# Performance work log

Hardware: AMD Instinct MI355X
Metric: run time of the kernel (lower is better)

The kernel has to match this reference:

```python
import jax, jax.numpy as jnp
import numpy as np

N_NODES = 50000
N_EDGES = 800000
IN_DIM = 256
HID = 32
HEADS = 8
OUT_DIM = 16
NEG_SLOPE = 0.2


def setup_inputs() -> dict:
    key = jax.random.key(0)
    ks = jax.random.split(key, 12)
    s = 0.05
    return {
        "emb": jax.random.normal(ks[0], (N_NODES, IN_DIM), jnp.float32),
        "src": jax.random.randint(ks[1], (N_EDGES,), 0, N_NODES),
        "dst": jax.random.randint(ks[2], (N_EDGES,), 0, N_NODES),
        "W1": jax.random.normal(ks[3], (IN_DIM, HEADS * HID), jnp.float32) * s,
        "attn_l1": jax.random.normal(ks[4], (HEADS, HID), jnp.float32) * s,
        "attn_r1": jax.random.normal(ks[5], (HEADS, HID), jnp.float32) * s,
        "bias1": jax.random.normal(ks[6], (HEADS * HID,), jnp.float32) * s,
        "W2": jax.random.normal(ks[7], (HEADS * HID, OUT_DIM), jnp.float32) * s,
        "attn_l2": jax.random.normal(ks[8], (1, OUT_DIM), jnp.float32) * s,
        "attn_r2": jax.random.normal(ks[9], (1, OUT_DIM), jnp.float32) * s,
        "bias2": jax.random.normal(ks[10], (OUT_DIM,), jnp.float32) * s,
    }


def gat_conv(x, src, dst, W, attn_l, attn_r, bias, n_heads, d_out):
    # x: [N, F_in] -> per-head projection h: [N, H, D]
    n = x.shape[0]
    h = (x @ W).reshape(n, n_heads, d_out)
    el = jnp.sum(h * attn_l, axis=-1)  # [N, H]
    er = jnp.sum(h * attn_r, axis=-1)  # [N, H]
    # edge scores with LeakyReLU (DGL negative_slope=0.2)
    e = jax.nn.leaky_relu(el[src] + er[dst], NEG_SLOPE)  # [E, H]
    # edge softmax over incoming edges of each destination node
    m = jax.ops.segment_max(e, dst, num_segments=n)  # [N, H]
    ee = jnp.exp(e - m[dst])
    denom = jax.ops.segment_sum(ee, dst, num_segments=n)  # [N, H]
    alpha = ee / denom[dst]  # [E, H]
    # weighted scatter-sum aggregation
    out = jax.ops.segment_sum(h[src] * alpha[:, :, None], dst, num_segments=n)  # [N, H, D]
    return out + bias.reshape(1, n_heads, d_out)


def reference(emb, src, dst, W1, attn_l1, attn_r1, bias1, W2, attn_l2, attn_r2, bias2):
    h = gat_conv(emb, src, dst, W1, attn_l1, attn_r1, bias1, HEADS, HID)  # [N, 8, 32]
    h = jax.nn.elu(h.reshape(N_NODES, HEADS * HID))  # [N, 256]
    out = gat_conv(h, src, dst, W2, attn_l2, attn_r2, bias2, 1, OUT_DIM)  # [N, 1, 16]
    return jnp.squeeze(out, axis=1)  # [N, 16]
```

## Files before the change

kernel.cpp:

```cpp
#include <hip/hip_runtime.h>
#include <math.h>

#define N_NODES 50000
#define N_EDGES 800000
#define NEG_SLOPE 0.2f

typedef __attribute__((ext_vector_type(8))) short bf16x8;
typedef __attribute__((ext_vector_type(4))) float f32x4;
typedef __attribute__((ext_vector_type(4))) _Float16 half4;

__device__ inline unsigned short f32_to_bf16_rn(float x) {
    unsigned u = __builtin_bit_cast(unsigned, x);
    unsigned r = u + 0x7fffu + ((u >> 16) & 1u);
    return (unsigned short)(r >> 16);
}
__device__ inline float bf16_bits_to_f32(unsigned short h) {
    unsigned u = ((unsigned)h) << 16;
    return __builtin_bit_cast(float, u);
}
__device__ inline void load_lds16(const void* g, void* l) {
    __builtin_amdgcn_global_load_lds(
        (const __attribute__((address_space(1))) void*)g,
        (__attribute__((address_space(3))) void*)l, 16, 0, 0);
}


__device__ __forceinline__ void count_body(int bb, const int* __restrict__ dst,
                                           int* __restrict__ deg) {
    int i = bb * 256 + threadIdx.x;
    if (i < N_EDGES) atomicAdd(&deg[dst[i]], 1);
}

__device__ __forceinline__ void convert_body(int n, const float* __restrict__ W,
                                             unsigned short* __restrict__ Th,
                                             unsigned short* __restrict__ Tl) {
    int k = threadIdx.x;
    float x = W[k * 256 + n];
    unsigned short h = f32_to_bf16_rn(x);
    float lo = x - bf16_bits_to_f32(h);
    size_t idx = ((size_t)(k >> 3) * 256 + n) * 8 + (k & 7);
    Th[idx] = h;
    Tl[idx] = f32_to_bf16_rn(lo);
}

__device__ __forceinline__ void assign_body(int bb, const int* __restrict__ deg,
                                            int* __restrict__ offs,
                                            int* __restrict__ cursor,
                                            int* __restrict__ gcounter) {
    __shared__ int buf[256];
    __shared__ int base;
    int tid = threadIdx.x;
    int v = bb * 256 + tid;
    int d = (v < N_NODES) ? deg[v] : 0;
    buf[tid] = d;
    __syncthreads();
    for (int off = 1; off < 256; off <<= 1) {
        int x = (tid >= off) ? buf[tid - off] : 0;
        __syncthreads();
        buf[tid] += x;
        __syncthreads();
    }
    if (tid == 255) base = atomicAdd(gcounter, buf[255]);
    __syncthreads();
    if (v < N_NODES) {
        int start = base + buf[tid] - d;
        offs[v] = start;
        cursor[v] = start;
    }
}

__device__ __forceinline__ void scatter_body(int bb, const int* __restrict__ src,
                                             const int* __restrict__ dst,
                                             int* __restrict__ cursor,
                                             int* __restrict__ src_csr) {
    int i = bb * 256 + threadIdx.x;
    if (i < N_EDGES) {
        int p = atomicAdd(&cursor[dst[i]], 1);
        src_csr[p] = src[i];
    }
}


__device__ __forceinline__ void gemm1_body(int bb, const float* __restrict__ A,
                                           const unsigned short* __restrict__ BTh,
                                           const unsigned short* __restrict__ BTl,
                                           const float* __restrict__ al,
                                           const float* __restrict__ ar,
                                           _Float16* __restrict__ C,
                                           float* __restrict__ el,
                                           float* __restrict__ er, int M) {
    __shared__ unsigned short Ah[4][64][8], Al[4][64][8];
    __shared__ unsigned short Bh[4][256][8], Bl[4][256][8];
    int tid = threadIdx.x;
    int lane = tid & 63, wave = tid >> 6;
    int kgl = lane >> 4, rl = lane & 15;
    int row0 = bb * 64;

    f32x4 acc[4][4];
#pragma unroll
    for (int i = 0; i < 4; i++)
#pragma unroll
        for (int j = 0; j < 4; j++) acc[i][j] = (f32x4){0.f, 0.f, 0.f, 0.f};

    int rowA = tid >> 2, kgA = tid & 3;
    int grA = row0 + rowA;
    const float* pA = &A[(size_t)grA * 256 + kgA * 8];
    float4 x0 = make_float4(0.f, 0.f, 0.f, 0.f);
    float4 x1 = make_float4(0.f, 0.f, 0.f, 0.f);
    if (grA < M) {
        x0 = *reinterpret_cast<const float4*>(pA);
        x1 = *reinterpret_cast<const float4*>(pA + 4);
    }

    for (int step = 0; step < 8; step++) {
        int k0 = step * 32;
        {
            float xs[8] = {x0.x, x0.y, x0.z, x0.w, x1.x, x1.y, x1.z, x1.w};
            unsigned short hs[8], ls[8];
#pragma unroll
            for (int j = 0; j < 8; j++) {
                hs[j] = f32_to_bf16_rn(xs[j]);
                ls[j] = f32_to_bf16_rn(xs[j] - bf16_bits_to_f32(hs[j]));
            }
            *reinterpret_cast<bf16x8*>(&Ah[kgA][rowA][0]) = *reinterpret_cast<bf16x8*>(hs);
            *reinterpret_cast<bf16x8*>(&Al[kgA][rowA][0]) = *reinterpret_cast<bf16x8*>(ls);
        }
        int s0 = k0 >> 3;
#pragma unroll
        for (int i = 0; i < 4; i++) {
            load_lds16(&BTh[((size_t)(s0 + i) * 256 + tid) * 8], &Bh[i][wave << 6][0]);
            load_lds16(&BTl[((size_t)(s0 + i) * 256 + tid) * 8], &Bl[i][wave << 6][0]);
        }
        __syncthreads();
        if (step < 7 && grA < M) {
            x0 = *reinterpret_cast<const float4*>(pA + (step + 1) * 32);
            x1 = *reinterpret_cast<const float4*>(pA + (step + 1) * 32 + 4);
        }
        bf16x8 a_h[4], a_l[4];
#pragma unroll
        for (int mf = 0; mf < 4; mf++) {
            int row = mf * 16 + rl;
            a_h[mf] = *reinterpret_cast<bf16x8*>(&Ah[kgl][row][0]);
            a_l[mf] = *reinterpret_cast<bf16x8*>(&Al[kgl][row][0]);
        }
#pragma unroll
        for (int nf = 0; nf < 4; nf++) {
            int col = wave * 64 + nf * 16 + rl;
            bf16x8 bh = *reinterpret_cast<bf16x8*>(&Bh[kgl][col][0]);
            bf16x8 bl = *reinterpret_cast<bf16x8*>(&Bl[kgl][col][0]);
#pragma unroll
            for (int mf = 0; mf < 4; mf++) {
                acc[mf][nf] = __builtin_amdgcn_mfma_f32_16x16x32_bf16(a_h[mf], bh, acc[mf][nf], 0, 0, 0);
                acc[mf][nf] = __builtin_amdgcn_mfma_f32_16x16x32_bf16(a_h[mf], bl, acc[mf][nf], 0, 0, 0);
                acc[mf][nf] = __builtin_amdgcn_mfma_f32_16x16x32_bf16(a_l[mf], bh, acc[mf][nf], 0, 0, 0);
            }
        }
        __syncthreads();
    }
    float alv[4], arv[4];
#pragma unroll
    for (int nf = 0; nf < 4; nf++) {
        int c = wave * 64 + nf * 16 + rl;
        alv[nf] = al[c];
        arv[nf] = ar[c];
    }
#pragma unroll
    for (int mf = 0; mf < 4; mf++) {
#pragma unroll
        for (int rr = 0; rr < 4; rr++) {
            int grow = row0 + mf * 16 + (lane >> 4) * 4 + rr;
            bool ok = grow < M;
            if (ok) {
#pragma unroll
                for (int nf = 0; nf < 4; nf++) {
                    int gcol = wave * 64 + nf * 16 + rl;
                    C[(size_t)grow * 256 + gcol] = (_Float16)acc[mf][nf][rr];
                }
            }
            float e0 = acc[mf][0][rr] * alv[0] + acc[mf][1][rr] * alv[1];
            float e1 = acc[mf][2][rr] * alv[2] + acc[mf][3][rr] * alv[3];
            float f0 = acc[mf][0][rr] * arv[0] + acc[mf][1][rr] * arv[1];
            float f1 = acc[mf][2][rr] * arv[2] + acc[mf][3][rr] * arv[3];
#pragma unroll
            for (int off = 8; off >= 1; off >>= 1) {
                e0 += __shfl_down(e0, off, 16);
                e1 += __shfl_down(e1, off, 16);
                f0 += __shfl_down(f0, off, 16);
                f1 += __shfl_down(f1, off, 16);
            }
            if (rl == 0 && ok) {
                int h0 = wave * 2;
                el[grow * 8 + h0] = e0;
                el[grow * 8 + h0 + 1] = e1;
                er[grow * 8 + h0] = f0;
                er[grow * 8 + h0 + 1] = f1;
            }
        }
    }
}


__global__ __launch_bounds__(256) void k_count_convert(const int* __restrict__ dst,
                                                       int* __restrict__ deg,
                                                       const float* __restrict__ W1,
                                                       unsigned short* __restrict__ Th,
                                                       unsigned short* __restrict__ Tl) {
    int b = blockIdx.x;
    if (b < 3125) count_body(b, dst, deg);
    else convert_body(b - 3125, W1, Th, Tl);
}

__global__ __launch_bounds__(256) void k_gemmA_assign(const float* __restrict__ A,
                                                      const unsigned short* __restrict__ BTh,
                                                      const unsigned short* __restrict__ BTl,
                                                      const float* __restrict__ al,
                                                      const float* __restrict__ ar,
                                                      _Float16* __restrict__ C,
                                                      float* __restrict__ el,
                                                      float* __restrict__ er, int M,
                                                      const int* __restrict__ deg,
                                                      int* __restrict__ offs,
                                                      int* __restrict__ cursor,
                                                      int* __restrict__ gcounter) {
    int b = blockIdx.x;
    if (b < 391) gemm1_body(b, A, BTh, BTl, al, ar, C, el, er, M);
    else assign_body(b - 391, deg, offs, cursor, gcounter);
}

__global__ __launch_bounds__(256) void k_gemmB_scatter(const float* __restrict__ A,
                                                       const unsigned short* __restrict__ BTh,
                                                       const unsigned short* __restrict__ BTl,
                                                       const float* __restrict__ al,
                                                       const float* __restrict__ ar,
                                                       _Float16* __restrict__ C,
                                                       float* __restrict__ el,
                                                       float* __restrict__ er, int M,
                                                       const int* __restrict__ src,
                                                       const int* __restrict__ dst,
                                                       int* __restrict__ cursor,
                                                       int* __restrict__ src_csr) {
    int b = blockIdx.x;
    if (b < 391) gemm1_body(391 + b, A, BTh, BTl, al, ar, C, el, er, M);
    else scatter_body(b - 391, src, dst, cursor, src_csr);
}


__global__ __launch_bounds__(64) void agg1_fused(const int* __restrict__ offs,
                                                 const int* __restrict__ deg_arr,
                                                 const int* __restrict__ src_csr,
                                                 const float* __restrict__ el,
                                                 const float* __restrict__ er,
                                                 const _Float16* __restrict__ h1h,
                                                 const float* __restrict__ bias1,
                                                 _Float16* __restrict__ x2) {
    __shared__ float sc[64][8];
    int v = blockIdx.x;
    int t = threadIdx.x;
    int head = t >> 3, slot = t & 7;
    int start = offs[v];
    int deg = deg_arr[v];
    int end = start + deg;
    int ncache = (deg < 64) ? deg : 64;
    float erv = er[v * 8 + head];
    float s = 0.f;
    for (int base = 0; base < ncache; base += 8) {
        int e = base + slot;
        if (e < ncache) {
            int u = src_csr[start + e];
            float x = el[u * 8 + head] + erv;
            x = (x >= 0.f) ? x : NEG_SLOPE * x;
            float ex = expf(x);
            sc[e][head] = ex;
            s += ex;
        }
    }
    for (int base = 64; base < deg; base += 8) {
        int e = base + slot;
        if (e < deg) {
            int u = src_csr[start + e];
            float x = el[u * 8 + head] + erv;
            x = (x >= 0.f) ? x : NEG_SLOPE * x;
            s += expf(x);
        }
    }
    s += __shfl_xor(s, 1);
    s += __shfl_xor(s, 2);
    s += __shfl_xor(s, 4);
    float invs = (s > 0.f) ? 1.f / s : 0.f;
    __syncthreads();
    float4 acc = make_float4(0.f, 0.f, 0.f, 0.f);
    int i = start;
    for (; i + 3 < end && (i - start) + 3 < 64; i += 4) {
        int e = i - start;
        int u0 = src_csr[i];
        int u1 = src_csr[i + 1];
        int u2 = src_csr[i + 2];
        int u3 = src_csr[i + 3];
        float a0 = sc[e][head] * invs;
        float a1 = sc[e + 1][head] * invs;
        float a2 = sc[e + 2][head] * invs;
        float a3 = sc[e + 3][head] * invs;
        half4 p0 = *reinterpret_cast<const half4*>(&h1h[(size_t)u0 * 256 + 4 * t]);
        half4 p1 = *reinterpret_cast<const half4*>(&h1h[(size_t)u1 * 256 + 4 * t]);
        half4 p2 = *reinterpret_cast<const half4*>(&h1h[(size_t)u2 * 256 + 4 * t]);
        half4 p3 = *reinterpret_cast<const half4*>(&h1h[(size_t)u3 * 256 + 4 * t]);
        acc.x += a0 * (float)p0[0] + a1 * (float)p1[0] + a2 * (float)p2[0] + a3 * (float)p3[0];
        acc.y += a0 * (float)p0[1] + a1 * (float)p1[1] + a2 * (float)p2[1] + a3 * (float)p3[1];
        acc.z += a0 * (float)p0[2] + a1 * (float)p1[2] + a2 * (float)p2[2] + a3 * (float)p3[2];
        acc.w += a0 * (float)p0[3] + a1 * (float)p1[3] + a2 * (float)p2[3] + a3 * (float)p3[3];
    }
    for (; i < end; i++) {
        int e = i - start;
        int u0 = src_csr[i];
        float a0;
        if (e < 64) {
            a0 = sc[e][head] * invs;
        } else {
            float x = el[u0 * 8 + head] + erv;
            x = (x >= 0.f) ? x : NEG_SLOPE * x;
            a0 = expf(x) * invs;
        }
        half4 p0 = *reinterpret_cast<const half4*>(&h1h[(size_t)u0 * 256 + 4 * t]);
        acc.x += a0 * (float)p0[0];
        acc.y += a0 * (float)p0[1];
        acc.z += a0 * (float)p0[2];
        acc.w += a0 * (float)p0[3];
    }
    float4 b = *reinterpret_cast<const float4*>(&bias1[4 * t]);
    float ox = acc.x + b.x, oy = acc.y + b.y, oz = acc.z + b.z, ow = acc.w + b.w;
    ox = (ox > 0.f) ? ox : (expf(ox) - 1.f);
    oy = (oy > 0.f) ? oy : (expf(oy) - 1.f);
    oz = (oz > 0.f) ? oz : (expf(oz) - 1.f);
    ow = (ow > 0.f) ? ow : (expf(ow) - 1.f);
    half4 o = {(_Float16)ox, (_Float16)oy, (_Float16)oz, (_Float16)ow};
    *reinterpret_cast<half4*>(&x2[(size_t)v * 256 + 4 * t]) = o;
}


__global__ __launch_bounds__(256) void gemm2_mfma(const _Float16* __restrict__ X,
                                                  const float* __restrict__ W2,
                                                  const float* __restrict__ al,
                                                  const float* __restrict__ ar,
                                                  _Float16* __restrict__ h2,
                                                  float* __restrict__ el2,
                                                  float* __restrict__ er2, int M) {
    __shared__ unsigned short Xh[16][64][8], Xl[16][64][8];
    __shared__ unsigned short Wh[32][16][8], Wl[32][16][8];
    int tid = threadIdx.x;
    int lane = tid & 63, wave = tid >> 6;
    int kgl = lane >> 4, rl = lane & 15;
    int row0 = blockIdx.x * 64;

#pragma unroll
    for (int j = 0; j < 16; j++) {
        int e = tid * 16 + j;
        float x = W2[e];
        unsigned short h = f32_to_bf16_rn(x);
        unsigned short l = f32_to_bf16_rn(x - bf16_bits_to_f32(h));
        int k = e >> 4, c = e & 15;
        Wh[k >> 3][c][k & 7] = h;
        Wl[k >> 3][c][k & 7] = l;
    }

    f32x4 acc = (f32x4){0.f, 0.f, 0.f, 0.f};
    int rowX = tid >> 2, kgb = (tid & 3) * 4;
    int grX = row0 + rowX;
    for (int step = 0; step < 2; step++) {
#pragma unroll
        for (int j = 0; j < 4; j++) {
            int kg = kgb + j;
            int kglob = step * 128 + kg * 8;
            unsigned short hs[8], ls[8];
            if (grX < M) {
                half4 a0 = *reinterpret_cast<const half4*>(&X[(size_t)grX * 256 + kglob]);
                half4 a1 = *reinterpret_cast<const half4*>(&X[(size_t)grX * 256 + kglob + 4]);
                float xs[8] = {(float)a0[0], (float)a0[1], (float)a0[2], (float)a0[3],
                               (float)a1[0], (float)a1[1], (float)a1[2], (float)a1[3]};
#pragma unroll
                for (int q = 0; q < 8; q++) {
                    hs[q] = f32_to_bf16_rn(xs[q]);
                    ls[q] = f32_to_bf16_rn(xs[q] - bf16_bits_to_f32(hs[q]));
                }
            } else {
#pragma unroll
                for (int q = 0; q < 8; q++) { hs[q] = 0; ls[q] = 0; }
            }
            *reinterpret_cast<bf16x8*>(&Xh[kg][rowX][0]) = *reinterpret_cast<bf16x8*>(hs);
            *reinterpret_cast<bf16x8*>(&Xl[kg][rowX][0]) = *reinterpret_cast<bf16x8*>(ls);
        }
        __syncthreads();
#pragma unroll
        for (int ks = 0; ks < 4; ks++) {
            int kg = ks * 4 + kgl;
            int kgw = step * 16 + kg;
            bf16x8 a_h = *reinterpret_cast<bf16x8*>(&Xh[kg][wave * 16 + rl][0]);
            bf16x8 a_l = *reinterpret_cast<bf16x8*>(&Xl[kg][wave * 16 + rl][0]);
            bf16x8 b_h = *reinterpret_cast<bf16x8*>(&Wh[kgw][rl][0]);
            bf16x8 b_l = *reinterpret_cast<bf16x8*>(&Wl[kgw][rl][0]);
            acc = __builtin_amdgcn_mfma_f32_16x16x32_bf16(a_h, b_h, acc, 0, 0, 0);
            acc = __builtin_amdgcn_mfma_f32_16x16x32_bf16(a_h, b_l, acc, 0, 0, 0);
            acc = __builtin_amdgcn_mfma_f32_16x16x32_bf16(a_l, b_h, acc, 0, 0, 0);
        }
        __syncthreads();
    }
    float alv = al[rl], arv = ar[rl];
#pragma unroll
    for (int rr = 0; rr < 4; rr++) {
        int grow = row0 + wave * 16 + (lane >> 4) * 4 + rr;
        bool ok = grow < M;
        if (ok) h2[(size_t)grow * 16 + rl] = (_Float16)acc[rr];
        float pl = acc[rr] * alv;
        float pr = acc[rr] * arv;
#pragma unroll
        for (int off = 8; off >= 1; off >>= 1) {
            pl += __shfl_down(pl, off, 16);
            pr += __shfl_down(pr, off, 16);
        }
        if (rl == 0 && ok) {
            el2[grow] = pl;
            er2[grow] = pr;
        }
    }
}


__global__ __launch_bounds__(64) void agg2_fused(const int* __restrict__ offs,
                                                 const int* __restrict__ deg_arr,
                                                 const int* __restrict__ src_csr,
                                                 const float* __restrict__ el2,
                                                 const float* __restrict__ er2,
                                                 const _Float16* __restrict__ h2,
                                                 const float* __restrict__ bias2,
                                                 float* __restrict__ out) {
    __shared__ float sc2[64];
    int v = blockIdx.x;
    int t = threadIdx.x;
    int start = offs[v];
    int deg = deg_arr[v];
    int end = start + deg;
    int ncache = (deg < 64) ? deg : 64;
    float erv = er2[v];
    float s = 0.f;
    for (int e = t; e < ncache; e += 64) {
        int u = src_csr[start + e];
        float x = el2[u] + erv;
        x = (x >= 0.f) ? x : NEG_SLOPE * x;
        float ex = expf(x);
        sc2[e] = ex;
        s += ex;
    }
    for (int e = 64 + t; e < deg; e += 64) {
        int u = src_csr[start + e];
        float x = el2[u] + erv;
        x = (x >= 0.f) ? x : NEG_SLOPE * x;
        s += expf(x);
    }
#pragma unroll
    for (int off = 32; off >= 1; off >>= 1) s += __shfl_xor(s, off);
    float invs = (s > 0.f) ? 1.f / s : 0.f;
    __syncthreads();
    int eg = t >> 4, d = t & 15;
    float acc = 0.f;
    for (int i = start + eg; i < end; i += 4) {
        int e = i - start;
        int u = src_csr[i];
        float a;
        if (e < 64) {
            a = sc2[e] * invs;
        } else {
            float x = el2[u] + erv;
            x = (x >= 0.f) ? x : NEG_SLOPE * x;
            a = expf(x) * invs;
        }
        acc += a * (float)h2[(size_t)u * 16 + d];
    }
    acc += __shfl_xor(acc, 32);
    acc += __shfl_xor(acc, 16);
    if (t < 16) out[(size_t)v * 16 + t] = acc + bias2[t];
}


extern "C" void kernel_launch(void* const* d_in, const int* in_sizes, int n_in,
                              void* d_out, int out_size, void* d_ws, size_t ws_size,
                              hipStream_t stream) {
    const float* emb   = (const float*)d_in[0];
    const int*   src   = (const int*)d_in[1];
    const int*   dst   = (const int*)d_in[2];
    const float* W1    = (const float*)d_in[3];
    const float* al1   = (const float*)d_in[4];
    const float* ar1   = (const float*)d_in[5];
    const float* bias1 = (const float*)d_in[6];
    const float* W2    = (const float*)d_in[7];
    const float* al2   = (const float*)d_in[8];
    const float* ar2   = (const float*)d_in[9];
    const float* bias2 = (const float*)d_in[10];
    float* out = (float*)d_out;

    char* ws = (char*)d_ws;
    auto alloc = [&](size_t bytes) -> void* {
        void* p = ws;
        ws += (bytes + 255) & ~(size_t)255;
        return p;
    };
    int* deg     = (int*)alloc((N_NODES + 64) * 4);
    int* gcounter = deg + N_NODES;
    int* cursor  = (int*)alloc(N_NODES * 4);
    int* offs    = (int*)alloc(N_NODES * 4);
    int* src_csr = (int*)alloc(N_EDGES * 4);
    unsigned short* W1Th = (unsigned short*)alloc(256 * 256 * 2);
    unsigned short* W1Tl = (unsigned short*)alloc(256 * 256 * 2);
    _Float16* h1h = (_Float16*)alloc((size_t)N_NODES * 256 * 2);
    float* el1   = (float*)alloc(N_NODES * 8 * 4);
    float* er1   = (float*)alloc(N_NODES * 8 * 4);
    _Float16* x2h = (_Float16*)alloc((size_t)N_NODES * 256 * 2);
    _Float16* h2h = (_Float16*)alloc((size_t)N_NODES * 16 * 2);
    float* el2   = (float*)alloc(N_NODES * 4);
    float* er2   = (float*)alloc(N_NODES * 4);

    hipMemsetAsync(deg, 0, (N_NODES + 1) * 4, stream);
    k_count_convert<<<3381, 256, 0, stream>>>(dst, deg, W1, W1Th, W1Tl);
    k_gemmA_assign<<<587, 256, 0, stream>>>(emb, W1Th, W1Tl, al1, ar1, h1h, el1, er1,
                                            N_NODES, deg, offs, cursor, gcounter);
    k_gemmB_scatter<<<3516, 256, 0, stream>>>(emb, W1Th, W1Tl, al1, ar1, h1h, el1, er1,
                                              N_NODES, src, dst, cursor, src_csr);
    agg1_fused<<<N_NODES, 64, 0, stream>>>(offs, deg, src_csr, el1, er1, h1h, bias1, x2h);
    gemm2_mfma<<<(N_NODES + 63) / 64, 256, 0, stream>>>(x2h, W2, al2, ar2, h2h, el2, er2, N_NODES);
    agg2_fused<<<N_NODES, 64, 0, stream>>>(offs, deg, src_csr, el2, er2, h2h, bias2, out);
}
```

Baseline: 221.0 us.

## Fold layer-2 attention logits into agg1 and compute softmax denominators alongside gemm2

Precomputes W2·attn_l2 and W2·attn_r2 as 256-vectors so agg1 can emit el2/er2 directly from the fp32 ELU output, removing that dependence on the gemm2 result. The layer-2 softmax denominator pass then runs as extra blocks co-scheduled with gemm2, and agg2 becomes a single gather pass that recomputes exp per edge. This moves work off the serial agg2 critical path, at the cost of an extra reduction in agg1, an extra pass over edges, and redundant exp in agg2. Because el2/er2 now come from unrounded activations rather than the fp16-stored h2, values differ slightly from before.

```diff
diff --git a/kernel.cpp b/kernel.cpp
--- a/kernel.cpp
+++ b/kernel.cpp
@@ -41,6 +41,23 @@
     size_t idx = ((size_t)(k >> 3) * 256 + n) * 8 + (k & 7);
     Th[idx] = h;
     Tl[idx] = f32_to_bf16_rn(lo);
+}
+
+__device__ __forceinline__ void wvec_body(const float* __restrict__ W2,
+                                          const float* __restrict__ al2,
+                                          const float* __restrict__ ar2,
+                                          float* __restrict__ wal,
+                                          float* __restrict__ war) {
+    int k = threadIdx.x;
+    float a = 0.f, r = 0.f;
+#pragma unroll
+    for (int c = 0; c < 16; c++) {
+        float w = W2[k * 16 + c];
+        a += w * al2[c];
+        r += w * ar2[c];
+    }
+    wal[k] = a;
+    war[k] = r;
 }
 
 __device__ __forceinline__ void assign_body(int bb, const int* __restrict__ deg,
@@ -80,6 +97,31 @@
     }
 }
 
+__device__ __forceinline__ void score2_body(int bb, const int* __restrict__ offs,
+                                            const int* __restrict__ deg_arr,
+                                            const int* __restrict__ src_csr,
+                                            const float* __restrict__ el2,
+                                            const float* __restrict__ er2,
+                                            float* __restrict__ invs) {
+    int t = threadIdx.x;
+    int v = bb * 32 + (t >> 3);
+    int lane8 = t & 7;
+    if (v >= N_NODES) return;
+    int start = offs[v], dg = deg_arr[v];
+    float erv = er2[v];
+    float s = 0.f;
+    for (int e = lane8; e < dg; e += 8) {
+        int u = src_csr[start + e];
+        float x = el2[u] + erv;
+        x = (x >= 0.f) ? x : NEG_SLOPE * x;
+        s += expf(x);
+    }
+    s += __shfl_xor(s, 1);
+    s += __shfl_xor(s, 2);
+    s += __shfl_xor(s, 4);
+    if (lane8 == 0) invs[v] = (s > 0.f) ? 1.f / s : 0.f;
+}
+
 
 __device__ __forceinline__ void gemm1_body(int bb, const float* __restrict__ A,
                                            const unsigned short* __restrict__ BTh,
@@ -200,14 +242,90 @@
 }
 
 
+__device__ __forceinline__ void gemm2_body(int bb, const _Float16* __restrict__ X,
+                                           const float* __restrict__ W2,
+                                           _Float16* __restrict__ h2, int M) {
+    __shared__ unsigned short Xh[16][64][8], Xl[16][64][8];
+    __shared__ unsigned short Wh[32][16][8], Wl[32][16][8];
+    int tid = threadIdx.x;
+    int lane = tid & 63, wave = tid >> 6;
+    int kgl = lane >> 4, rl = lane & 15;
+    int row0 = bb * 64;
+
+#pragma unroll
+    for (int j = 0; j < 16; j++) {
+        int e = tid * 16 + j;
+        float x = W2[e];
+        unsigned short h = f32_to_bf16_rn(x);
+        unsigned short l = f32_to_bf16_rn(x - bf16_bits_to_f32(h));
+        int k = e >> 4, c = e & 15;
+        Wh[k >> 3][c][k & 7] = h;
+        Wl[k >> 3][c][k & 7] = l;
+    }
+
+    f32x4 acc = (f32x4){0.f, 0.f, 0.f, 0.f};
+    int rowX = tid >> 2, kgb = (tid & 3) * 4;
+    int grX = row0 + rowX;
+    for (int step = 0; step < 2; step++) {
+#pragma unroll
+        for (int j = 0; j < 4; j++) {
+            int kg = kgb + j;
+            int kglob = step * 128 + kg * 8;
+            unsigned short hs[8], ls[8];
+            if (grX < M) {
+                half4 a0 = *reinterpret_cast<const half4*>(&X[(size_t)grX * 256 + kglob]);
+                half4 a1 = *reinterpret_cast<const half4*>(&X[(size_t)grX * 256 + kglob + 4]);
+                float xs[8] = {(float)a0[0], (float)a0[1], (float)a0[2], (float)a0[3],
+                               (float)a1[0], (float)a1[1], (float)a1[2], (float)a1[3]};
+#pragma unroll
+                for (int q = 0; q < 8; q++) {
+                    hs[q] = f32_to_bf16_rn(xs[q]);
+                    ls[q] = f32_to_bf16_rn(xs[q] - bf16_bits_to_f32(hs[q]));
+                }
+            } else {
+#pragma unroll
+                for (int q = 0; q < 8; q++) { hs[q] = 0; ls[q] = 0; }
+            }
+            *reinterpret_cast<bf16x8*>(&Xh[kg][rowX][0]) = *reinterpret_cast<bf16x8*>(hs);
+            *reinterpret_cast<bf16x8*>(&Xl[kg][rowX][0]) = *reinterpret_cast<bf16x8*>(ls);
+        }
+        __syncthreads();
+#pragma unroll
+        for (int ks = 0; ks < 4; ks++) {
+            int kg = ks * 4 + kgl;
+            int kgw = step * 16 + kg;
+            bf16x8 a_h = *reinterpret_cast<bf16x8*>(&Xh[kg][wave * 16 + rl][0]);
+            bf16x8 a_l = *reinterpret_cast<bf16x8*>(&Xl[kg][wave * 16 + rl][0]);
+            bf16x8 b_h = *reinterpret_cast<bf16x8*>(&Wh[kgw][rl][0]);
+            bf16x8 b_l = *reinterpret_cast<bf16x8*>(&Wl[kgw][rl][0]);
+            acc = __builtin_amdgcn_mfma_f32_16x16x32_bf16(a_h, b_h, acc, 0, 0, 0);
+            acc = __builtin_amdgcn_mfma_f32_16x16x32_bf16(a_h, b_l, acc, 0, 0, 0);
+            acc = __builtin_amdgcn_mfma_f32_16x16x32_bf16(a_l, b_h, acc, 0, 0, 0);
+        }
+        __syncthreads();
+    }
+#pragma unroll
+    for (int rr = 0; rr < 4; rr++) {
+        int grow = row0 + wave * 16 + (lane >> 4) * 4 + rr;
+        if (grow < M) h2[(size_t)grow * 16 + rl] = (_Float16)acc[rr];
+    }
+}
+
+
 __global__ __launch_bounds__(256) void k_count_convert(const int* __restrict__ dst,
                                                        int* __restrict__ deg,
                                                        const float* __restrict__ W1,
                                                        unsigned short* __restrict__ Th,
-                                                       unsigned short* __restrict__ Tl) {
+                                                       unsigned short* __restrict__ Tl,
+                                                       const float* __restrict__ W2,
+                                                       const float* __restrict__ al2,
+                                                       const float* __restrict__ ar2,
+                                                       float* __restrict__ wal,
+                                                       float* __restrict__ war) {
     int b = blockIdx.x;
     if (b < 3125) count_body(b, dst, deg);
-    else convert_body(b - 3125, W1, Th, Tl);
+    else if (b < 3381) convert_body(b - 3125, W1, Th, Tl);
+    else wvec_body(W2, al2, ar2, wal, war);
 }
 
 __global__ __launch_bounds__(256) void k_gemmA_assign(const float* __restrict__ A,
@@ -244,6 +362,20 @@
     else scatter_body(b - 391, src, dst, cursor, src_csr);
 }
 
+__global__ __launch_bounds__(256) void k_gemm2_score(const _Float16* __restrict__ X,
+                                                     const float* __restrict__ W2,
+                                                     _Float16* __restrict__ h2, int M,
+                                                     const int* __restrict__ offs,
+                                                     const int* __restrict__ deg_arr,
+                                                     const int* __restrict__ src_csr,
+                                                     const float* __restrict__ el2,
+                                                     const float* __restrict__ er2,
+                                                     float* __restrict__ invs) {
+    int b = blockIdx.x;
+    if (b < 782) gemm2_body(b, X, W2, h2, M);
+    else score2_body(b - 782, offs, deg_arr, src_csr, el2, er2, invs);
+}
+
 
 __global__ __launch_bounds__(64) void agg1_fused(const int* __restrict__ offs,
                                                  const int* __restrict__ deg_arr,
@@ -252,7 +384,11 @@
                                                  const float* __restrict__ er,
                                                  const _Float16* __restrict__ h1h,
                                                  const float* __restrict__ bias1,
-                                                 _Float16* __restrict__ x2) {
+                                                 const float* __restrict__ wal,
+                                                 const float* __restrict__ war,
+                                                 _Float16* __restrict__ x2,
+                                                 float* __restrict__ el2,
+                                                 float* __restrict__ er2) {
     __shared__ float sc[64][8];
     int v = blockIdx.x;
     int t = threadIdx.x;
@@ -334,145 +470,45 @@
     ow = (ow > 0.f) ? ow : (expf(ow) - 1.f);
     half4 o = {(_Float16)ox, (_Float16)oy, (_Float16)oz, (_Float16)ow};
     *reinterpret_cast<half4*>(&x2[(size_t)v * 256 + 4 * t]) = o;
-}
-
-
-__global__ __launch_bounds__(256) void gemm2_mfma(const _Float16* __restrict__ X,
-                                                  const float* __restrict__ W2,
-                                                  const float* __restrict__ al,
-                                                  const float* __restrict__ ar,
-                                                  _Float16* __restrict__ h2,
-                                                  float* __restrict__ el2,
-                                                  float* __restrict__ er2, int M) {
-    __shared__ unsigned short Xh[16][64][8], Xl[16][64][8];
-    __shared__ unsigned short Wh[32][16][8], Wl[32][16][8];
-    int tid = threadIdx.x;
-    int lane = tid & 63, wave = tid >> 6;
-    int kgl = lane >> 4, rl = lane & 15;
-    int row0 = blockIdx.x * 64;
-
-#pragma unroll
-    for (int j = 0; j < 16; j++) {
-        int e = tid * 16 + j;
-        float x = W2[e];
-        unsigned short h = f32_to_bf16_rn(x);
-        unsigned short l = f32_to_bf16_rn(x - bf16_bits_to_f32(h));
-        int k = e >> 4, c = e & 15;
-        Wh[k >> 3][c][k & 7] = h;
-        Wl[k >> 3][c][k & 7] = l;
-    }
-
-    f32x4 acc = (f32x4){0.f, 0.f, 0.f, 0.f};
-    int rowX = tid >> 2, kgb = (tid & 3) * 4;
-    int grX = row0 + rowX;
-    for (int step = 0; step < 2; step++) {
-#pragma unroll
-        for (int j = 0; j < 4; j++) {
-            int kg = kgb + j;
-            int kglob = step * 128 + kg * 8;
-            unsigned short hs[8], ls[8];
-            if (grX < M) {
-                half4 a0 = *reinterpret_cast<const half4*>(&X[(size_t)grX * 256 + kglob]);
-                half4 a1 = *reinterpret_cast<const half4*>(&X[(size_t)grX * 256 + kglob + 4]);
-                float xs[8] = {(float)a0[0], (float)a0[1], (float)a0[2], (float)a0[3],
-                               (float)a1[0], (float)a1[1], (float)a1[2], (float)a1[3]};
-#pragma unroll
-                for (int q = 0; q < 8; q++) {
-                    hs[q] = f32_to_bf16_rn(xs[q]);
-                    ls[q] = f32_to_bf16_rn(xs[q] - bf16_bits_to_f32(hs[q]));
-                }
-            } else {
-#pragma unroll
-                for (int q = 0; q < 8; q++) { hs[q] = 0; ls[q] = 0; }
-            }
-            *reinterpret_cast<bf16x8*>(&Xh[kg][rowX][0]) = *reinterpret_cast<bf16x8*>(hs);
-            *reinterpret_cast<bf16x8*>(&Xl[kg][rowX][0]) = *reinterpret_cast<bf16x8*>(ls);
-        }
-        __syncthreads();
-#pragma unroll
-        for (int ks = 0; ks < 4; ks++) {
-            int kg = ks * 4 + kgl;
-            int kgw = step * 16 + kg;
-            bf16x8 a_h = *reinterpret_cast<bf16x8*>(&Xh[kg][wave * 16 + rl][0]);
-            bf16x8 a_l = *reinterpret_cast<bf16x8*>(&Xl[kg][wave * 16 + rl][0]);
-            bf16x8 b_h = *reinterpret_cast<bf16x8*>(&Wh[kgw][rl][0]);
-            bf16x8 b_l = *reinterpret_cast<bf16x8*>(&Wl[kgw][rl][0]);
-            acc = __builtin_amdgcn_mfma_f32_16x16x32_bf16(a_h, b_h, acc, 0, 0, 0);
-            acc = __builtin_amdgcn_mfma_f32_16x16x32_bf16(a_h, b_l, acc, 0, 0, 0);
-            acc = __builtin_amdgcn_mfma_f32_16x16x32_bf16(a_l, b_h, acc, 0, 0, 0);
-        }
-        __syncthreads();
-    }
-    float alv = al[rl], arv = ar[rl];
-#pragma unroll
-    for (int rr = 0; rr < 4; rr++) {
-        int grow = row0 + wave * 16 + (lane >> 4) * 4 + rr;
-        bool ok = grow < M;
-        if (ok) h2[(size_t)grow * 16 + rl] = (_Float16)acc[rr];
-        float pl = acc[rr] * alv;
-        float pr = acc[rr] * arv;
-#pragma unroll
-        for (int off = 8; off >= 1; off >>= 1) {
-            pl += __shfl_down(pl, off, 16);
-            pr += __shfl_down(pr, off, 16);
-        }
-        if (rl == 0 && ok) {
-            el2[grow] = pl;
-            er2[grow] = pr;
-        }
-    }
-}
-
-
-__global__ __launch_bounds__(64) void agg2_fused(const int* __restrict__ offs,
-                                                 const int* __restrict__ deg_arr,
-                                                 const int* __restrict__ src_csr,
-                                                 const float* __restrict__ el2,
-                                                 const float* __restrict__ er2,
-                                                 const _Float16* __restrict__ h2,
-                                                 const float* __restrict__ bias2,
-                                                 float* __restrict__ out) {
-    __shared__ float sc2[64];
+    float4 wa = *reinterpret_cast<const float4*>(&wal[4 * t]);
+    float4 wr = *reinterpret_cast<const float4*>(&war[4 * t]);
+    float pl = ox * wa.x + oy * wa.y + oz * wa.z + ow * wa.w;
+    float pr = ox * wr.x + oy * wr.y + oz * wr.z + ow * wr.w;
+#pragma unroll
+    for (int off = 32; off >= 1; off >>= 1) {
+        pl += __shfl_xor(pl, off);
+        pr += __shfl_xor(pr, off);
+    }
+    if (t == 0) {
+        el2[v] = pl;
+        er2[v] = pr;
+    }
+}
+
+
+__global__ __launch_bounds__(64) void agg2_gather(const int* __restrict__ offs,
+                                                  const int* __restrict__ deg_arr,
+                                                  const int* __restrict__ src_csr,
+                                                  const float* __restrict__ el2,
+                                                  const float* __restrict__ er2,
+                                                  const float* __restrict__ invs_g,
+                                                  const _Float16* __restrict__ h2,
+                                                  const float* __restrict__ bias2,
+                                                  float* __restrict__ out) {
     int v = blockIdx.x;
     int t = threadIdx.x;
     int start = offs[v];
     int deg = deg_arr[v];
     int end = start + deg;
-    int ncache = (deg < 64) ? deg : 64;
     float erv = er2[v];
-    float s = 0.f;
-    for (int e = t; e < ncache; e += 64) {
-        int u = src_csr[start + e];
-        float x = el2[u] + erv;
-        x = (x >= 0.f) ? x : NEG_SLOPE * x;
-        float ex = expf(x);
-        sc2[e] = ex;
-        s += ex;
-    }
-    for (int e = 64 + t; e < deg; e += 64) {
-        int u = src_csr[start + e];
-        float x = el2[u] + erv;
-        x = (x >= 0.f) ? x : NEG_SLOPE * x;
-        s += expf(x);
-    }
-#pragma unroll
-    for (int off = 32; off >= 1; off >>= 1) s += __shfl_xor(s, off);
-    float invs = (s > 0.f) ? 1.f / s : 0.f;
-    __syncthreads();
+    float iv = invs_g[v];
     int eg = t >> 4, d = t & 15;
     float acc = 0.f;
     for (int i = start + eg; i < end; i += 4) {
-        int e = i - start;
         int u = src_csr[i];
-        float a;
-        if (e < 64) {
-            a = sc2[e] * invs;
-        } else {
-            float x = el2[u] + erv;
-            x = (x >= 0.f) ? x : NEG_SLOPE * x;
-            a = expf(x) * invs;
-        }
-        acc += a * (float)h2[(size_t)u * 16 + d];
+        float x = el2[u] + erv;
+        x = (x >= 0.f) ? x : NEG_SLOPE * x;
+        acc += expf(x) * iv * (float)h2[(size_t)u * 16 + d];
     }
     acc += __shfl_xor(acc, 32);
     acc += __shfl_xor(acc, 16);
@@ -516,14 +552,21 @@
     _Float16* h2h = (_Float16*)alloc((size_t)N_NODES * 16 * 2);
     float* el2   = (float*)alloc(N_NODES * 4);
     float* er2   = (float*)alloc(N_NODES * 4);
+    float* invs  = (float*)alloc(N_NODES * 4);
+    float* wal   = (float*)alloc(256 * 4);
+    float* war   = (float*)alloc(256 * 4);
 
     hipMemsetAsync(deg, 0, (N_NODES + 1) * 4, stream);
-    k_count_convert<<<3381, 256, 0, stream>>>(dst, deg, W1, W1Th, W1Tl);
+    k_count_convert<<<3382, 256, 0, stream>>>(dst, deg, W1, W1Th, W1Tl,
+                                              W2, al2, ar2, wal, war);
     k_gemmA_assign<<<587, 256, 0, stream>>>(emb, W1Th, W1Tl, al1, ar1, h1h, el1, er1,
                                             N_NODES, deg, offs, cursor, gcounter);
     k_gemmB_scatter<<<3516, 256, 0, stream>>>(emb, W1Th, W1Tl, al1, ar1, h1h, el1, er1,
                                               N_NODES, src, dst, cursor, src_csr);
-    agg1_fused<<<N_NODES, 64, 0, stream>>>(offs, deg, src_csr, el1, er1, h1h, bias1, x2h);
-    gemm2_mfma<<<(N_NODES + 63) / 64, 256, 0, stream>>>(x2h, W2, al2, ar2, h2h, el2, er2, N_NODES);
-    agg2_fused<<<N_NODES, 64, 0, stream>>>(offs, deg, src_csr, el2, er2, h2h, bias2, out);
-}
+    agg1_fused<<<N_NODES, 64, 0, stream>>>(offs, deg, src_csr, el1, er1, h1h, bias1,
+                                           wal, war, x2h, el2, er2);
+    k_gemm2_score<<<2345, 256, 0, stream>>>(x2h, W2, h2h, N_NODES,
+                                            offs, deg, src_csr, el2, er2, invs);
+    agg2_gather<<<N_NODES, 64, 0, stream>>>(offs, deg, src_csr, el2, er2, invs,
+                                            h2h, bias2, out);
+}
```

Result: no change. 222.0 us (+0.4%).
